# Kernel tuning notes

Measured on AMD Instinct MI355X. Metric: run time of the kernel, lower is better.

The kernel has to match this reference:

```python
import jax, jax.numpy as jnp
import numpy as np

D_MODEL = 1024
NUM_HEADS = 16
D_K = D_MODEL // NUM_HEADS
TEMPERATURE = 1.0
LN_EPS = 1e-5


def setup_inputs() -> dict:
    key = jax.random.key(0)
    ks = jax.random.split(key, 12)
    B, S, D = 4, 1024, D_MODEL
    w = lambda k: jax.random.normal(k, (D, D), dtype=jnp.float32) * 0.02
    b = lambda k: jax.random.normal(k, (D,), dtype=jnp.float32) * 0.01
    return {
        "query": jax.random.normal(ks[0], (B, S, D), dtype=jnp.float32),
        "key": jax.random.normal(ks[1], (B, S, D), dtype=jnp.float32),
        "value": jax.random.normal(ks[2], (B, S, D), dtype=jnp.float32),
        "wq": w(ks[3]), "bq": b(ks[4]),
        "wk": w(ks[5]), "bk": b(ks[6]),
        "wv": w(ks[7]), "bv": b(ks[8]),
        "wo": w(ks[9]), "bo": b(ks[10]),
        "temporal_bias": jax.random.normal(ks[11], (1, 1, NUM_HEADS, 1, 1), dtype=jnp.float32) * 0.01,
        "adaptive_temp": jnp.ones((1,), dtype=jnp.float32),
        "ln_gamma": jnp.ones((D,), dtype=jnp.float32),
        "ln_beta": jnp.zeros((D,), dtype=jnp.float32),
    }


def reference(query, key, value, wq, bq, wk, bk, wv, bv, wo, bo,
              temporal_bias, adaptive_temp, ln_gamma, ln_beta):
    B, S, D = query.shape
    H, dk = NUM_HEADS, D_K
    # QKV projections -> (B, H, S, dk)
    Q = (query @ wq.T + bq).reshape(B, S, H, dk).transpose(0, 2, 1, 3)
    K = (key @ wk.T + bk).reshape(B, S, H, dk).transpose(0, 2, 1, 3)
    V = (value @ wv.T + bv).reshape(B, S, H, dk).transpose(0, 2, 1, 3)
    scores = jnp.einsum('bhqd,bhkd->bhqk', Q, K) / jnp.sqrt(jnp.float32(dk))
    scores = scores / (TEMPERATURE * adaptive_temp)
    # torch broadcasting bug reproduced: (B,H,S,S) + (1,1,H,1,1) -> (1,B,H,S,S)
    scores5 = scores[None, ...] + temporal_bias  # (1, B, H, S, S)
    attn = jax.nn.softmax(scores5, axis=-1)      # (1, B, H, S, S)
    ctx5 = jnp.einsum('xbhqk,bhkd->xbhqd', attn, V)  # (1, B, H, S, dk)
    # torch: transpose(1,2) -> (1, H, B, S, dk), then view(B, S, D)
    ctx = jnp.swapaxes(ctx5, 1, 2).reshape(B, S, D)
    out = ctx @ wo.T + bo
    y = out + query
    mu = jnp.mean(y, axis=-1, keepdims=True)
    var = jnp.mean(jnp.square(y - mu), axis=-1, keepdims=True)
    out_ln = (y - mu) / jnp.sqrt(var + LN_EPS) * ln_gamma + ln_beta
    return out_ln, attn
```

## Files before the change

### kernel.cpp

```cpp
#include <hip/hip_runtime.h>
#include <math.h>

#define BB 4
#define SS 1024
#define DD 1024
#define HH 16
#define DKK 64
#define NN (BB*SS)
#define LN_EPS 1e-5f
#define QB 128
#define JB 64

typedef __attribute__((ext_vector_type(8))) short bf16x8;
typedef __attribute__((ext_vector_type(4))) float f32x4;
typedef __attribute__((address_space(3))) unsigned int lds_u32;
typedef const __attribute__((address_space(1))) unsigned int glb_u32;

static __device__ __forceinline__ unsigned short f2bf(float x){
    unsigned int u = __float_as_uint(x);
    u += 0x7fff + ((u >> 16) & 1);
    return (unsigned short)(u >> 16);
}
static __device__ __forceinline__ int swzp(int q){
    return ((q & 7) << 4) ^ ((q & 8) << 2);
}

__global__ __launch_bounds__(256)
void k_cvt_all(const float* __restrict__ q, const float* __restrict__ k,
               const float* __restrict__ v, const float* __restrict__ w0,
               const float* __restrict__ w1, const float* __restrict__ w2,
               const float* __restrict__ w3, unsigned short* __restrict__ xout,
               unsigned short* __restrict__ wout){
    const int bidx = blockIdx.x;
    const float* src; unsigned short* dst; size_t i;
    if (bidx < 6144) {
        const int z = bidx >> 11, bi = bidx & 2047;
        src = (z == 0) ? q : (z == 1) ? k : v;
        dst = xout + (size_t)z*NN*DD;
        i = ((size_t)bi*256 + threadIdx.x)*8;
    } else {
        const int z = (bidx - 6144) >> 9, bi = (bidx - 6144) & 511;
        src = (z == 0) ? w0 : (z == 1) ? w1 : (z == 2) ? w2 : w3;
        dst = wout + (size_t)z*DD*DD;
        i = ((size_t)bi*256 + threadIdx.x)*8;
    }
    float4 a = *reinterpret_cast<const float4*>(&src[i]);
    float4 b = *reinterpret_cast<const float4*>(&src[i+4]);
    int4 w;
    w.x = (int)((unsigned)f2bf(a.x) | ((unsigned)f2bf(a.y) << 16));
    w.y = (int)((unsigned)f2bf(a.z) | ((unsigned)f2bf(a.w) << 16));
    w.z = (int)((unsigned)f2bf(b.x) | ((unsigned)f2bf(b.y) << 16));
    w.w = (int)((unsigned)f2bf(b.z) | ((unsigned)f2bf(b.w) << 16));
    *reinterpret_cast<int4*>(&dst[i]) = w;
}

__global__ __launch_bounds__(256)
void k_gemmqkv(const unsigned short* __restrict__ Xb, const unsigned short* __restrict__ Wb,
               const float* __restrict__ b0, const float* __restrict__ b1,
               const float* __restrict__ b2, unsigned short* __restrict__ outb)
{
    __shared__ __align__(16) unsigned short Als[128*32];
    __shared__ __align__(16) unsigned short Bls[128*32];
    __shared__ __align__(16) unsigned short Cs[128*128];
    const int z = blockIdx.z;
    const unsigned short* X = Xb + (size_t)z*NN*DD;
    const unsigned short* W = Wb + (size_t)z*DD*DD;
    const float* bias = (z == 0) ? b0 : (z == 1) ? b1 : b2;
    unsigned short* out = outb + (size_t)z*NN*DD;

    const int row0 = blockIdx.x * 128;
    const int col0 = blockIdx.y * 128;
    const int t = threadIdx.x;
    const int w = t >> 6, l = t & 63;
    const int wr = w >> 1, wc = w & 1;

    f32x4 acc[4][4];
    #pragma unroll
    for (int m=0;m<4;++m)
        #pragma unroll
        for (int n=0;n<4;++n) acc[m][n] = (f32x4){0.f,0.f,0.f,0.f};

    const int srow  = l >> 2;
    const int skoff = (l & 3) * 8;

    for (int kt = 0; kt < DD; kt += 32) {
        #pragma unroll
        for (int i=0;i<2;++i) {
            const unsigned short* ga = X + (size_t)(row0 + w*32 + i*16 + srow)*DD + kt + skoff;
            const unsigned short* gb = W + (size_t)(col0 + w*32 + i*16 + srow)*DD + kt + skoff;
            __builtin_amdgcn_global_load_lds((glb_u32*)ga, (lds_u32*)&Als[(w*2+i)*512], 16, 0, 0);
            __builtin_amdgcn_global_load_lds((glb_u32*)gb, (lds_u32*)&Bls[(w*2+i)*512], 16, 0, 0);
        }
        __syncthreads();
        bf16x8 af[4], bfr[4];
        #pragma unroll
        for (int m=0;m<4;++m)
            af[m] = *reinterpret_cast<const bf16x8*>(&Als[(wr*64 + m*16 + (l&15))*32 + (l>>4)*8]);
        #pragma unroll
        for (int n=0;n<4;++n)
            bfr[n] = *reinterpret_cast<const bf16x8*>(&Bls[(wc*64 + n*16 + (l&15))*32 + (l>>4)*8]);
        __builtin_amdgcn_s_setprio(1);
        #pragma unroll
        for (int m=0;m<4;++m)
            #pragma unroll
            for (int n=0;n<4;++n)
                acc[m][n] = __builtin_amdgcn_mfma_f32_16x16x32_bf16(af[m], bfr[n], acc[m][n], 0, 0, 0);
        __builtin_amdgcn_s_setprio(0);
        __syncthreads();
    }

    if (z < 2) {
        #pragma unroll
        for (int m=0;m<4;++m){
            const int trb = wr*64 + m*16 + ((l>>4)<<2);
            #pragma unroll
            for (int n=0;n<4;++n){
                const int tc = wc*64 + n*16 + (l&15);
                const float bc = bias[col0 + tc];
                #pragma unroll
                for (int r=0;r<4;++r){
                    const int tr = trb + r;
                    *reinterpret_cast<unsigned short*>(
                        (char*)Cs + ((tr*256 + tc*2) ^ ((tr & 12) << 3))) = f2bf(acc[m][n][r] + bc);
                }
            }
        }
        __syncthreads();
        #pragma unroll
        for (int i=0;i<8;++i){
            const int slot = i*256 + t;
            const int r2 = slot >> 4, g = slot & 15;
            int4 v = *reinterpret_cast<const int4*>(
                (char*)Cs + ((r2*256 + g*16) ^ ((r2 & 12) << 3)));
            *reinterpret_cast<int4*>(&out[(size_t)(row0 + r2)*DD + col0 + g*8]) = v;
        }
    } else {
        #pragma unroll
        for (int m=0;m<4;++m){
            const int trb = wr*64 + m*16 + ((l>>4)<<2);
            #pragma unroll
            for (int n=0;n<4;++n){
                const int tc = wc*64 + n*16 + (l&15);
                const float bc = bias[col0 + tc];
                ushort4 pk;
                pk.x = f2bf(acc[m][n][0] + bc);
                pk.y = f2bf(acc[m][n][1] + bc);
                pk.z = f2bf(acc[m][n][2] + bc);
                pk.w = f2bf(acc[m][n][3] + bc);
                *reinterpret_cast<ushort4*>(
                    (char*)Cs + ((tc*256 + trb*2) ^ ((tc & 15) << 3))) = pk;
            }
        }
        __syncthreads();
        const int b = row0 >> 10;
        const int sbase = row0 & 1023;
        #pragma unroll
        for (int i=0;i<16;++i){
            const int cr = i*8 + (t>>5);
            const int ch = t & 31;
            ushort4 v = *reinterpret_cast<const ushort4*>(
                (char*)Cs + ((cr*256 + ch*8) ^ ((cr & 15) << 3)));
            const int gc = col0 + cr, h = gc >> 6, k = gc & 63;
            *reinterpret_cast<ushort4*>(
                &out[(((size_t)b*HH + h)*DKK + k)*SS + sbase + ch*4]) = v;
        }
    }
}

__global__ __launch_bounds__(512)
void k_attn(const unsigned short* __restrict__ Qb, const unsigned short* __restrict__ Kb,
            const unsigned short* __restrict__ Vtb, const float* __restrict__ at,
            float* __restrict__ attn, unsigned short* __restrict__ ctxb)
{
    __shared__ __align__(16) unsigned short Qs[QB*64];
    __shared__ __align__(16) unsigned short Ks[JB*64];
    __shared__ __align__(16) unsigned short Vs[DKK*JB];
    __shared__ __align__(16) unsigned short Ps[QB*JB];
    const int f   = blockIdx.x;
    const int wk2 = (f & 7)*64 + (f >> 3);
    const int bh  = wk2 >> 3;
    const int q0  = (wk2 & 7) * QB;
    const int b = bh >> 4, h = bh & 15;
    const int t = threadIdx.x, w = t >> 6, l = t & 63;
    const float alpha = 0.125f / at[0];

    const unsigned short* Qg = Qb  + (size_t)b*SS*DD + (size_t)h*64;
    const unsigned short* Kg = Kb  + (size_t)b*SS*DD + (size_t)h*64;
    const unsigned short* Vg = Vtb + (size_t)bh*DKK*SS;

    const int sj  = t >> 3;
    const int skc = (t & 7) * 8;

    #pragma unroll
    for (int p = 0; p < 2; ++p) {
        const int c = t + p*512;
        const int q = c >> 3, kc = (c & 7) * 8;
        int4 v = *reinterpret_cast<const int4*>(&Qg[(size_t)(q0 + q)*DD + kc]);
        *reinterpret_cast<int4*>((char*)Qs + ((q*128 + kc*2) ^ ((q & 7) << 4))) = v;
    }
    {
        int4 kv = *reinterpret_cast<const int4*>(&Kg[(size_t)sj*DD + skc]);
        *reinterpret_cast<int4*>((char*)Ks + ((sj*128 + skc*2) ^ ((sj & 7) << 4))) = kv;
    }
    __syncthreads();
    bf16x8 qf[2];
    {
        const int q = w*16 + (l & 15);
        #pragma unroll
        for (int ks = 0; ks < 2; ++ks)
            qf[ks] = *reinterpret_cast<const bf16x8*>(
                (char*)Qs + ((q*128 + (l>>4)*16 + ks*64) ^ ((q & 7) << 4)));
    }

    float m[4], s[4];
    #pragma unroll
    for (int r = 0; r < 4; ++r) { m[r] = -1e30f; s[r] = 0.f; }

    for (int j0 = 0; j0 < SS; j0 += JB) {
        int4 knext;
        if (j0 + JB < SS)
            knext = *reinterpret_cast<const int4*>(&Kg[(size_t)(j0 + JB + sj)*DD + skc]);
        f32x4 acc[4];
        #pragma unroll
        for (int n = 0; n < 4; ++n) acc[n] = (f32x4){0.f,0.f,0.f,0.f};
        __builtin_amdgcn_s_setprio(1);
        #pragma unroll
        for (int ks = 0; ks < 2; ++ks) {
            #pragma unroll
            for (int n = 0; n < 4; ++n) {
                const int j = n*16 + (l & 15);
                bf16x8 kf = *reinterpret_cast<const bf16x8*>(
                    (char*)Ks + ((j*128 + (l>>4)*16 + ks*64) ^ ((j & 7) << 4)));
                acc[n] = __builtin_amdgcn_mfma_f32_16x16x32_bf16(qf[ks], kf, acc[n], 0, 0, 0);
            }
        }
        __builtin_amdgcn_s_setprio(0);
        #pragma unroll
        for (int r = 0; r < 4; ++r) {
            float tm = fmaxf(fmaxf(acc[0][r], acc[1][r]), fmaxf(acc[2][r], acc[3][r])) * alpha;
            #pragma unroll
            for (int off = 1; off < 16; off <<= 1)
                tm = fmaxf(tm, __shfl_xor(tm, off, 64));
            const float mn = fmaxf(m[r], tm);
            float ps = __expf(acc[0][r]*alpha - mn) + __expf(acc[1][r]*alpha - mn)
                     + __expf(acc[2][r]*alpha - mn) + __expf(acc[3][r]*alpha - mn);
            #pragma unroll
            for (int off = 1; off < 16; off <<= 1)
                ps += __shfl_xor(ps, off, 64);
            s[r] = s[r] * __expf(m[r] - mn) + ps;
            m[r] = mn;
        }
        __syncthreads();
        if (j0 + JB < SS) {
            *reinterpret_cast<int4*>((char*)Ks + ((sj*128 + skc*2) ^ ((sj & 7) << 4))) = knext;
        }
        __syncthreads();
    }

    float sinv[4];
    #pragma unroll
    for (int r = 0; r < 4; ++r) sinv[r] = 1.0f / s[r];

    f32x4 cacc[4];
    #pragma unroll
    for (int n = 0; n < 4; ++n) cacc[n] = (f32x4){0.f,0.f,0.f,0.f};

    {
        int4 kv = *reinterpret_cast<const int4*>(&Kg[(size_t)sj*DD + skc]);
        int4 vv = *reinterpret_cast<const int4*>(&Vg[(size_t)sj*SS + skc]);
        *reinterpret_cast<int4*>((char*)Ks + ((sj*128 + skc*2) ^ ((sj & 7) << 4))) = kv;
        *reinterpret_cast<int4*>((char*)Vs + ((sj*128 + skc*2) ^ ((sj & 7) << 4))) = vv;
    }
    __syncthreads();

    for (int j0 = 0; j0 < SS; j0 += JB) {
        int4 knext, vnext;
        if (j0 + JB < SS) {
            knext = *reinterpret_cast<const int4*>(&Kg[(size_t)(j0 + JB + sj)*DD + skc]);
            vnext = *reinterpret_cast<const int4*>(&Vg[(size_t)sj*SS + j0 + JB + skc]);
        }
        f32x4 acc[4];
        #pragma unroll
        for (int n = 0; n < 4; ++n) acc[n] = (f32x4){0.f,0.f,0.f,0.f};
        __builtin_amdgcn_s_setprio(1);
        #pragma unroll
        for (int ks = 0; ks < 2; ++ks) {
            #pragma unroll
            for (int n = 0; n < 4; ++n) {
                const int j = n*16 + (l & 15);
                bf16x8 kf = *reinterpret_cast<const bf16x8*>(
                    (char*)Ks + ((j*128 + (l>>4)*16 + ks*64) ^ ((j & 7) << 4)));
                acc[n] = __builtin_amdgcn_mfma_f32_16x16x32_bf16(qf[ks], kf, acc[n], 0, 0, 0);
            }
        }
        __builtin_amdgcn_s_setprio(0);
        #pragma unroll
        for (int n = 0; n < 4; ++n) {
            const int jl = n*16 + (l & 15);
            #pragma unroll
            for (int r = 0; r < 4; ++r) {
                const int q = w*16 + (l>>4)*4 + r;
                const float p = __expf(acc[n][r]*alpha - m[r]) * sinv[r];
                *reinterpret_cast<unsigned short*>(
                    (char*)Ps + ((q*128 + jl*2) ^ swzp(q))) = f2bf(p);
            }
        }
        __syncthreads();
        __builtin_amdgcn_s_setprio(1);
        #pragma unroll
        for (int ks = 0; ks < 2; ++ks) {
            const int qr = w*16 + (l & 15);
            bf16x8 pf = *reinterpret_cast<const bf16x8*>(
                (char*)Ps + ((qr*128 + (l>>4)*16 + ks*64) ^ swzp(qr)));
            #pragma unroll
            for (int n = 0; n < 4; ++n) {
                const int d = n*16 + (l & 15);
                bf16x8 vf = *reinterpret_cast<const bf16x8*>(
                    (char*)Vs + ((d*128 + (l>>4)*16 + ks*64) ^ ((d & 7) << 4)));
                cacc[n] = __builtin_amdgcn_mfma_f32_16x16x32_bf16(pf, vf, cacc[n], 0, 0, 0);
            }
        }
        __builtin_amdgcn_s_setprio(0);
        #pragma unroll
        for (int i = 0; i < 4; ++i) {
            const int sr = i*32 + (t >> 4);
            const int j4 = (t & 15) * 4;
            int2 u = *reinterpret_cast<const int2*>(
                (char*)Ps + ((sr*128 + j4*2) ^ swzp(sr)));
            f32x4 fv;
            fv.x = __uint_as_float(((unsigned)u.x) << 16);
            fv.y = __uint_as_float(((unsigned)u.x) & 0xffff0000u);
            fv.z = __uint_as_float(((unsigned)u.y) << 16);
            fv.w = __uint_as_float(((unsigned)u.y) & 0xffff0000u);
            __builtin_nontemporal_store(fv, reinterpret_cast<f32x4*>(
                &attn[((size_t)bh*SS + q0 + sr)*SS + j0 + j4]));
        }
        __syncthreads();
        if (j0 + JB < SS) {
            *reinterpret_cast<int4*>((char*)Ks + ((sj*128 + skc*2) ^ ((sj & 7) << 4))) = knext;
            *reinterpret_cast<int4*>((char*)Vs + ((sj*128 + skc*2) ^ ((sj & 7) << 4))) = vnext;
        }
        __syncthreads();
    }

    #pragma unroll
    for (int n = 0; n < 4; ++n) {
        const int d = n*16 + (l & 15);
        #pragma unroll
        for (int r = 0; r < 4; ++r) {
            const int q = q0 + w*16 + (l>>4)*4 + r;
            ctxb[(((size_t)h*BB + b)*SS + q)*DKK + d] = f2bf(cacc[n][r]);
        }
    }
}

__global__ __launch_bounds__(256)
void k_gemmo(const unsigned short* __restrict__ X, const unsigned short* __restrict__ W,
             const float* __restrict__ bias, const float* __restrict__ resid,
             float* __restrict__ outf)
{
    __shared__ __align__(16) unsigned short Als[128*32];
    __shared__ __align__(16) unsigned short Bls[128*32];
    const int row0 = blockIdx.x * 128;
    const int col0 = blockIdx.y * 128;
    const int t = threadIdx.x;
    const int w = t >> 6, l = t & 63;
    const int wr = w >> 1, wc = w & 1;

    f32x4 acc[4][4];
    #pragma unroll
    for (int m=0;m<4;++m)
        #pragma unroll
        for (int n=0;n<4;++n) acc[m][n] = (f32x4){0.f,0.f,0.f,0.f};

    const int srow  = l >> 2;
    const int skoff = (l & 3) * 8;

    for (int kt = 0; kt < DD; kt += 32) {
        #pragma unroll
        for (int i=0;i<2;++i) {
            const unsigned short* ga = X + (size_t)(row0 + w*32 + i*16 + srow)*DD + kt + skoff;
            const unsigned short* gb = W + (size_t)(col0 + w*32 + i*16 + srow)*DD + kt + skoff;
            __builtin_amdgcn_global_load_lds((glb_u32*)ga, (lds_u32*)&Als[(w*2+i)*512], 16, 0, 0);
            __builtin_amdgcn_global_load_lds((glb_u32*)gb, (lds_u32*)&Bls[(w*2+i)*512], 16, 0, 0);
        }
        __syncthreads();
        bf16x8 af[4], bfr[4];
        #pragma unroll
        for (int m=0;m<4;++m)
            af[m] = *reinterpret_cast<const bf16x8*>(&Als[(wr*64 + m*16 + (l&15))*32 + (l>>4)*8]);
        #pragma unroll
        for (int n=0;n<4;++n)
            bfr[n] = *reinterpret_cast<const bf16x8*>(&Bls[(wc*64 + n*16 + (l&15))*32 + (l>>4)*8]);
        __builtin_amdgcn_s_setprio(1);
        #pragma unroll
        for (int m=0;m<4;++m)
            #pragma unroll
            for (int n=0;n<4;++n)
                acc[m][n] = __builtin_amdgcn_mfma_f32_16x16x32_bf16(af[m], bfr[n], acc[m][n], 0, 0, 0);
        __builtin_amdgcn_s_setprio(0);
        __syncthreads();
    }

    #pragma unroll
    for (int m=0;m<4;++m){
        const int grow_base = row0 + wr*64 + m*16 + ((l>>4)<<2);
        #pragma unroll
        for (int n=0;n<4;++n){
            const int col = col0 + wc*64 + n*16 + (l&15);
            const float bc = bias[col];
            #pragma unroll
            for (int r=0;r<4;++r){
                const int row = grow_base + r;
                outf[(size_t)row*DD + col] = acc[m][n][r] + bc + resid[(size_t)row*DD + col];
            }
        }
    }
}

__global__ __launch_bounds__(256)
void k_ln(const float* __restrict__ y, const float* __restrict__ g,
          const float* __restrict__ be, float* __restrict__ out)
{
    const int row = blockIdx.x;
    const int t = threadIdx.x;
    float4 v = *reinterpret_cast<const float4*>(&y[(size_t)row*DD + t*4]);
    float s  = v.x + v.y + v.z + v.w;
    float ss = v.x*v.x + v.y*v.y + v.z*v.z + v.w*v.w;
    #pragma unroll
    for (int off = 32; off > 0; off >>= 1) {
        s  += __shfl_xor(s,  off, 64);
        ss += __shfl_xor(ss, off, 64);
    }
    __shared__ float red[8];
    const int lane = t & 63, wid = t >> 6;
    if (lane == 0) { red[wid] = s; red[4+wid] = ss; }
    __syncthreads();
    const float S1 = red[0]+red[1]+red[2]+red[3];
    const float S2 = red[4]+red[5]+red[6]+red[7];
    const float mu  = S1 * (1.0f/DD);
    const float var = fmaxf(S2 * (1.0f/DD) - mu*mu, 0.0f);
    const float rstd = rsqrtf(var + LN_EPS);
    float4 gv = *reinterpret_cast<const float4*>(&g[t*4]);
    float4 bv = *reinterpret_cast<const float4*>(&be[t*4]);
    float4 o;
    o.x = (v.x - mu)*rstd*gv.x + bv.x;
    o.y = (v.y - mu)*rstd*gv.y + bv.y;
    o.z = (v.z - mu)*rstd*gv.z + bv.z;
    o.w = (v.w - mu)*rstd*gv.w + bv.w;
    *reinterpret_cast<float4*>(&out[(size_t)row*DD + t*4]) = o;
}

extern "C" void kernel_launch(void* const* d_in, const int* in_sizes, int n_in,
                              void* d_out, int out_size, void* d_ws, size_t ws_size,
                              hipStream_t stream) {
    const float* query = (const float*)d_in[0];
    const float* key   = (const float*)d_in[1];
    const float* value = (const float*)d_in[2];
    const float* wq = (const float*)d_in[3];
    const float* bq = (const float*)d_in[4];
    const float* wk = (const float*)d_in[5];
    const float* bk = (const float*)d_in[6];
    const float* wv = (const float*)d_in[7];
    const float* bv = (const float*)d_in[8];
    const float* wo = (const float*)d_in[9];
    const float* bo = (const float*)d_in[10];
    const float* at = (const float*)d_in[12];
    const float* g  = (const float*)d_in[13];
    const float* be = (const float*)d_in[14];

    float* out_ln = (float*)d_out;
    float* attn   = (float*)d_out + (size_t)NN*DD;

    char* wsb = (char*)d_ws;
    unsigned short* xq   = (unsigned short*)(wsb);
    unsigned short* Qb   = (unsigned short*)(wsb + ((size_t)24<<20));
    unsigned short* Kb   = (unsigned short*)(wsb + ((size_t)32<<20));
    unsigned short* Vtb  = (unsigned short*)(wsb + ((size_t)40<<20));
    unsigned short* ctxb = (unsigned short*)(wsb + ((size_t)48<<20));
    unsigned short* wqb  = (unsigned short*)(wsb + ((size_t)56<<20));
    float*          y    = (float*)(wsb);

    k_cvt_all<<<8192, 256, 0, stream>>>(query, key, value, wq, wk, wv, wo, xq, wqb);

    k_gemmqkv<<<dim3(32, 8, 3), 256, 0, stream>>>(xq, wqb, bq, bk, bv, Qb);

    k_attn<<<dim3(512), 512, 0, stream>>>(Qb, Kb, Vtb, at, attn, ctxb);

    k_gemmo<<<dim3(32, 8), 256, 0, stream>>>(ctxb, wqb + (size_t)3*DD*DD, bo, query, y);

    k_ln<<<NN, 256, 0, stream>>>(y, g, be, out_ln);
}
```

Baseline: 186.1 us.

## Double-buffer K/V tiles and transpose QK MFMA so rows stay within lanes

```diff
diff --git a/kernel.cpp b/kernel.cpp
--- a/kernel.cpp
+++ b/kernel.cpp
@@ -173,8 +173,8 @@
             float* __restrict__ attn, unsigned short* __restrict__ ctxb)
 {
     __shared__ __align__(16) unsigned short Qs[QB*64];
-    __shared__ __align__(16) unsigned short Ks[JB*64];
-    __shared__ __align__(16) unsigned short Vs[DKK*JB];
+    __shared__ __align__(16) unsigned short Ks[2][JB*64];
+    __shared__ __align__(16) unsigned short Vs[2][DKK*JB];
     __shared__ __align__(16) unsigned short Ps[QB*JB];
     const int f   = blockIdx.x;
     const int wk2 = (f & 7)*64 + (f >> 3);
@@ -200,7 +200,7 @@
     }
     {
         int4 kv = *reinterpret_cast<const int4*>(&Kg[(size_t)sj*DD + skc]);
-        *reinterpret_cast<int4*>((char*)Ks + ((sj*128 + skc*2) ^ ((sj & 7) << 4))) = kv;
+        *reinterpret_cast<int4*>((char*)Ks[0] + ((sj*128 + skc*2) ^ ((sj & 7) << 4))) = kv;
     }
     __syncthreads();
     bf16x8 qf[2];
@@ -212,13 +212,13 @@
                 (char*)Qs + ((q*128 + (l>>4)*16 + ks*64) ^ ((q & 7) << 4)));
     }
 
-    float m[4], s[4];
-    #pragma unroll
-    for (int r = 0; r < 4; ++r) { m[r] = -1e30f; s[r] = 0.f; }
-
+    float mrow = -1e30f, srow = 0.f;
+
+    int cur = 0;
     for (int j0 = 0; j0 < SS; j0 += JB) {
         int4 knext;
-        if (j0 + JB < SS)
+        const bool more = (j0 + JB < SS);
+        if (more)
             knext = *reinterpret_cast<const int4*>(&Kg[(size_t)(j0 + JB + sj)*DD + skc]);
         f32x4 acc[4];
         #pragma unroll
@@ -230,36 +230,35 @@
             for (int n = 0; n < 4; ++n) {
                 const int j = n*16 + (l & 15);
                 bf16x8 kf = *reinterpret_cast<const bf16x8*>(
-                    (char*)Ks + ((j*128 + (l>>4)*16 + ks*64) ^ ((j & 7) << 4)));
-                acc[n] = __builtin_amdgcn_mfma_f32_16x16x32_bf16(qf[ks], kf, acc[n], 0, 0, 0);
+                    (char*)Ks[cur] + ((j*128 + (l>>4)*16 + ks*64) ^ ((j & 7) << 4)));
+                acc[n] = __builtin_amdgcn_mfma_f32_16x16x32_bf16(kf, qf[ks], acc[n], 0, 0, 0);
             }
         }
         __builtin_amdgcn_s_setprio(0);
-        #pragma unroll
-        for (int r = 0; r < 4; ++r) {
-            float tm = fmaxf(fmaxf(acc[0][r], acc[1][r]), fmaxf(acc[2][r], acc[3][r])) * alpha;
-            #pragma unroll
-            for (int off = 1; off < 16; off <<= 1)
-                tm = fmaxf(tm, __shfl_xor(tm, off, 64));
-            const float mn = fmaxf(m[r], tm);
-            float ps = __expf(acc[0][r]*alpha - mn) + __expf(acc[1][r]*alpha - mn)
-                     + __expf(acc[2][r]*alpha - mn) + __expf(acc[3][r]*alpha - mn);
-            #pragma unroll
-            for (int off = 1; off < 16; off <<= 1)
-                ps += __shfl_xor(ps, off, 64);
-            s[r] = s[r] * __expf(m[r] - mn) + ps;
-            m[r] = mn;
-        }
-        __syncthreads();
-        if (j0 + JB < SS) {
-            *reinterpret_cast<int4*>((char*)Ks + ((sj*128 + skc*2) ^ ((sj & 7) << 4))) = knext;
-        }
-        __syncthreads();
-    }
-
-    float sinv[4];
-    #pragma unroll
-    for (int r = 0; r < 4; ++r) sinv[r] = 1.0f / s[r];
+        float a[16];
+        #pragma unroll
+        for (int n = 0; n < 4; ++n)
+            #pragma unroll
+            for (int r = 0; r < 4; ++r) a[n*4+r] = acc[n][r]*alpha;
+        float tm = a[0];
+        #pragma unroll
+        for (int i = 1; i < 16; ++i) tm = fmaxf(tm, a[i]);
+        tm = fmaxf(tm, __shfl_xor(tm, 16, 64));
+        tm = fmaxf(tm, __shfl_xor(tm, 32, 64));
+        const float mn = fmaxf(mrow, tm);
+        float ps = 0.f;
+        #pragma unroll
+        for (int i = 0; i < 16; ++i) ps += __expf(a[i] - mn);
+        ps += __shfl_xor(ps, 16, 64);
+        ps += __shfl_xor(ps, 32, 64);
+        srow = srow * __expf(mrow - mn) + ps;
+        mrow = mn;
+        if (more)
+            *reinterpret_cast<int4*>((char*)Ks[cur^1] + ((sj*128 + skc*2) ^ ((sj & 7) << 4))) = knext;
+        __syncthreads();
+        cur ^= 1;
+    }
+    const float sinv = 1.0f / srow;
 
     f32x4 cacc[4];
     #pragma unroll
@@ -268,14 +267,16 @@
     {
         int4 kv = *reinterpret_cast<const int4*>(&Kg[(size_t)sj*DD + skc]);
         int4 vv = *reinterpret_cast<const int4*>(&Vg[(size_t)sj*SS + skc]);
-        *reinterpret_cast<int4*>((char*)Ks + ((sj*128 + skc*2) ^ ((sj & 7) << 4))) = kv;
-        *reinterpret_cast<int4*>((char*)Vs + ((sj*128 + skc*2) ^ ((sj & 7) << 4))) = vv;
+        *reinterpret_cast<int4*>((char*)Ks[0] + ((sj*128 + skc*2) ^ ((sj & 7) << 4))) = kv;
+        *reinterpret_cast<int4*>((char*)Vs[0] + ((sj*128 + skc*2) ^ ((sj & 7) << 4))) = vv;
     }
     __syncthreads();
 
+    cur = 0;
     for (int j0 = 0; j0 < SS; j0 += JB) {
         int4 knext, vnext;
-        if (j0 + JB < SS) {
+        const bool more = (j0 + JB < SS);
+        if (more) {
             knext = *reinterpret_cast<const int4*>(&Kg[(size_t)(j0 + JB + sj)*DD + skc]);
             vnext = *reinterpret_cast<const int4*>(&Vg[(size_t)sj*SS + j0 + JB + skc]);
         }
@@ -289,21 +290,30 @@
             for (int n = 0; n < 4; ++n) {
                 const int j = n*16 + (l & 15);
                 bf16x8 kf = *reinterpret_cast<const bf16x8*>(
-                    (char*)Ks + ((j*128 + (l>>4)*16 + ks*64) ^ ((j & 7) << 4)));
-                acc[n] = __builtin_amdgcn_mfma_f32_16x16x32_bf16(qf[ks], kf, acc[n], 0, 0, 0);
+                    (char*)Ks[cur] + ((j*128 + (l>>4)*16 + ks*64) ^ ((j & 7) << 4)));
+                acc[n] = __builtin_amdgcn_mfma_f32_16x16x32_bf16(kf, qf[ks], acc[n], 0, 0, 0);
             }
         }
         __builtin_amdgcn_s_setprio(0);
-        #pragma unroll
-        for (int n = 0; n < 4; ++n) {
-            const int jl = n*16 + (l & 15);
-            #pragma unroll
-            for (int r = 0; r < 4; ++r) {
-                const int q = w*16 + (l>>4)*4 + r;
-                const float p = __expf(acc[n][r]*alpha - m[r]) * sinv[r];
-                *reinterpret_cast<unsigned short*>(
-                    (char*)Ps + ((q*128 + jl*2) ^ swzp(q))) = f2bf(p);
-            }
+        {
+            const int q = w*16 + (l & 15);
+            const int c = l >> 4;
+            #pragma unroll
+            for (int n = 0; n < 4; ++n) {
+                float p0 = __expf(acc[n][0]*alpha - mrow) * sinv;
+                float p1 = __expf(acc[n][1]*alpha - mrow) * sinv;
+                float p2 = __expf(acc[n][2]*alpha - mrow) * sinv;
+                float p3 = __expf(acc[n][3]*alpha - mrow) * sinv;
+                int2 pk;
+                pk.x = (int)((unsigned)f2bf(p0) | ((unsigned)f2bf(p1) << 16));
+                pk.y = (int)((unsigned)f2bf(p2) | ((unsigned)f2bf(p3) << 16));
+                *reinterpret_cast<int2*>(
+                    (char*)Ps + ((q*128 + n*32 + c*8) ^ swzp(q))) = pk;
+            }
+        }
+        if (more) {
+            *reinterpret_cast<int4*>((char*)Ks[cur^1] + ((sj*128 + skc*2) ^ ((sj & 7) << 4))) = knext;
+            *reinterpret_cast<int4*>((char*)Vs[cur^1] + ((sj*128 + skc*2) ^ ((sj & 7) << 4))) = vnext;
         }
         __syncthreads();
         __builtin_amdgcn_s_setprio(1);
@@ -316,7 +326,7 @@
             for (int n = 0; n < 4; ++n) {
                 const int d = n*16 + (l & 15);
                 bf16x8 vf = *reinterpret_cast<const bf16x8*>(
-                    (char*)Vs + ((d*128 + (l>>4)*16 + ks*64) ^ ((d & 7) << 4)));
+                    (char*)Vs[cur] + ((d*128 + (l>>4)*16 + ks*64) ^ ((d & 7) << 4)));
                 cacc[n] = __builtin_amdgcn_mfma_f32_16x16x32_bf16(pf, vf, cacc[n], 0, 0, 0);
             }
         }
@@ -336,11 +346,7 @@
                 &attn[((size_t)bh*SS + q0 + sr)*SS + j0 + j4]));
         }
         __syncthreads();
-        if (j0 + JB < SS) {
-            *reinterpret_cast<int4*>((char*)Ks + ((sj*128 + skc*2) ^ ((sj & 7) << 4))) = knext;
-            *reinterpret_cast<int4*>((char*)Vs + ((sj*128 + skc*2) ^ ((sj & 7) << 4))) = vnext;
-        }
-        __syncthreads();
+        cur ^= 1;
     }
 
     #pragma unroll
```

Measured after the change: 176.2 us. -5.3%, faster.
